# Performance work log

Measured on AMD Instinct MI355X. Metric: run time of the kernel, lower is better.

The kernel has to match this reference:

```python
import jax, jax.numpy as jnp
import numpy as np

BIG = 1e6  # diagonal mask value from the original module


def setup_inputs() -> dict:
    key = jax.random.key(0)
    k1, k2, k3 = jax.random.split(key, 3)
    B, D = 16384, 128
    return {
        "query_embeddings": jax.random.normal(k1, (B, D), dtype=jnp.float32),
        "doc_embeddings": jax.random.normal(k2, (B, D), dtype=jnp.float32),
        "neg_doc_embeddings": jax.random.normal(k3, (B, D), dtype=jnp.float32),
    }


def reference(query_embeddings, doc_embeddings, neg_doc_embeddings):
    # Pairwise term: diagonal of q @ d.T is just a row-wise dot product.
    pos_scores = jnp.einsum("bd,bd->b", query_embeddings, doc_embeddings)
    neg_scores = jnp.einsum("bd,bd->b", query_embeddings, neg_doc_embeddings)
    loss = jax.nn.softplus(neg_scores - pos_scores).mean()

    # In-batch hardest-negative term (in_batch_term=True): full [B, B] scores.
    scores = jnp.einsum("bd,cd->bc", query_embeddings, doc_embeddings)
    B = scores.shape[0]
    idx = jnp.arange(B)
    pos_ib = scores[idx, idx]
    # subtract 1e6 on the diagonal (same as original: scores - eye * 1e6)
    neg_ib = scores.at[idx, idx].add(-BIG).max(axis=1)
    loss = loss + jax.nn.softplus(neg_ib - pos_ib).mean()

    return loss / 2
```

## Files before the change

### kernel.cpp

```cpp
#include <hip/hip_runtime.h>
#include <hip/hip_bf16.h>


#define BATCH 16384
#define DDIM  128
#define NWAVES 8
#define ROWS_PER_BLOCK 512
#define COLS_PER_BLOCK 2048
#define CHUNK_COLS 128
#define NCHUNKS (COLS_PER_BLOCK / CHUNK_COLS)
#define CHUNK_USHORTS (CHUNK_COLS * DDIM)
#define NCG (BATCH / COLS_PER_BLOCK)

typedef __attribute__((ext_vector_type(8))) short bf16x8;
typedef __attribute__((ext_vector_type(4))) float f32x4;

__device__ __forceinline__ float softplus_f(float x) {
    return (x > 0.0f) ? x + log1pf(expf(-x)) : log1pf(expf(x));
}

__device__ __forceinline__ ushort f2bf_rne(float x) {
    unsigned u = __float_as_uint(x);
    unsigned r = (u + 0x7FFFu + ((u >> 16) & 1u)) >> 16;
    return (ushort)r;
}

#define WAITVM(n) do { \
        __builtin_amdgcn_s_waitcnt((n) | (7 << 4) | (15 << 8)); \
        asm volatile("" ::: "memory"); \
    } while (0)

__global__ __launch_bounds__(256) void prep_kernel(
    const float* __restrict__ q, const float* __restrict__ d,
    const float* __restrict__ nd,
    ushort* __restrict__ qb, ushort* __restrict__ db,
    float* __restrict__ pos, float* __restrict__ acc)
{
    const int t   = threadIdx.x;
    const int blk = blockIdx.x;
    const int sub = t >> 5;
    const int ln  = t & 31;
    const size_t base = (size_t)blk * (64 * DDIM);

    float loss1 = 0.0f;
#pragma unroll
    for (int i = 0; i < 8; ++i) {
        size_t idx = base + (size_t)i * 1024 + (size_t)t * 4;
        float4 a = *(const float4*)(q  + idx);
        float4 b = *(const float4*)(d  + idx);
        float4 c = *(const float4*)(nd + idx);

        ushort4 o;
        o.x = f2bf_rne(a.x); o.y = f2bf_rne(a.y);
        o.z = f2bf_rne(a.z); o.w = f2bf_rne(a.w);
        *(ushort4*)(qb + idx) = o;
        ushort4 p;
        p.x = f2bf_rne(b.x); p.y = f2bf_rne(b.y);
        p.z = f2bf_rne(b.z); p.w = f2bf_rne(b.w);
        *(ushort4*)(db + idx) = p;

        float ps = a.x * b.x + a.y * b.y + a.z * b.z + a.w * b.w;
        float ns = a.x * c.x + a.y * c.y + a.z * c.z + a.w * c.w;
        ps += __shfl_xor(ps, 1); ps += __shfl_xor(ps, 2);
        ps += __shfl_xor(ps, 4); ps += __shfl_xor(ps, 8);
        ps += __shfl_xor(ps, 16);
        ns += __shfl_xor(ns, 1); ns += __shfl_xor(ns, 2);
        ns += __shfl_xor(ns, 4); ns += __shfl_xor(ns, 8);
        ns += __shfl_xor(ns, 16);
        if (ln == 0) {
            int r = blk * 64 + i * 8 + sub;
            pos[r] = ps;
            loss1 += softplus_f(ns - ps);
        }
    }
    loss1 += __shfl_xor(loss1, 1);  loss1 += __shfl_xor(loss1, 2);
    loss1 += __shfl_xor(loss1, 4);  loss1 += __shfl_xor(loss1, 8);
    loss1 += __shfl_xor(loss1, 16); loss1 += __shfl_xor(loss1, 32);
    if ((t & 63) == 0) atomicAdd(acc, loss1);
}

__global__ __launch_bounds__(512, 2) void inbatch_kernel(
    const ushort* __restrict__ qb, const ushort* __restrict__ db,
    float* __restrict__ partials)
{
    __shared__ ushort stg[2][CHUNK_USHORTS];

    const int t      = threadIdx.x;
    const int w      = t >> 6;
    const int l      = t & 63;
    const int lane16 = l & 15;
    const int quad   = l >> 4;
    const int rg     = blockIdx.x & 31;
    const int cg     = blockIdx.x >> 5;
    const int rows0  = rg * ROWS_PER_BLOCK + w * 64;
    const int col0   = cg * COLS_PER_BLOCK;

    bf16x8 afrag[4][4];
#pragma unroll
    for (int rs = 0; rs < 4; ++rs)
#pragma unroll
        for (int ks = 0; ks < 4; ++ks)
            afrag[rs][ks] = *(const bf16x8*)(
                qb + (size_t)(rows0 + rs * 16 + lane16) * DDIM + ks * 32 + quad * 8);

    const ushort* gsrc[4];
#pragma unroll
    for (int i = 0; i < 4; ++i) {
        int seg = i * 512 + t;
        int c   = seg >> 4;
        int s   = seg & 15;
        gsrc[i] = db + (size_t)(col0 + c) * DDIM + ((s ^ (c & 15)) * 8);
    }

    int dsbase[4];
#pragma unroll
    for (int ks = 0; ks < 4; ++ks)
        dsbase[ks] = lane16 * DDIM + (((ks * 4 + quad) ^ lane16) * 8);

    float runmax[4][4];
#pragma unroll
    for (int rs = 0; rs < 4; ++rs)
#pragma unroll
        for (int r = 0; r < 4; ++r) runmax[rs][r] = -3.0e38f;

#pragma unroll
    for (int i = 0; i < 4; ++i)
        __builtin_amdgcn_global_load_lds(
            (const __attribute__((address_space(1))) void*)gsrc[i],
            (__attribute__((address_space(3))) void*)(&stg[0][0] + (i * 512 + w * 64) * 8),
            16, 0, 0);

    for (int ch = 0; ch < NCHUNKS; ++ch) {
        WAITVM(0);
        __syncthreads();
        if (ch + 1 < NCHUNKS) {
#pragma unroll
            for (int i = 0; i < 4; ++i)
                __builtin_amdgcn_global_load_lds(
                    (const __attribute__((address_space(1))) void*)(gsrc[i] + (size_t)(ch + 1) * CHUNK_USHORTS),
                    (__attribute__((address_space(3))) void*)(&stg[(ch + 1) & 1][0] + (i * 512 + w * 64) * 8),
                    16, 0, 0);
        }

        const ushort* buf = &stg[ch & 1][0];
#pragma unroll
        for (int ct = 0; ct < 8; ++ct) {
            bf16x8 bfrag[4];
#pragma unroll
            for (int ks = 0; ks < 4; ++ks)
                bfrag[ks] = *(const bf16x8*)(buf + dsbase[ks] + ct * 2048);

            const int ctile = col0 + ch * CHUNK_COLS + ct * 16;
#pragma unroll
            for (int rs = 0; rs < 4; ++rs) {
                f32x4 s = {0.0f, 0.0f, 0.0f, 0.0f};
#pragma unroll
                for (int ks = 0; ks < 4; ++ks)
                    s = __builtin_amdgcn_mfma_f32_16x16x32_bf16(
                        afrag[rs][ks], bfrag[ks], s, 0, 0, 0);
                if (ctile == rows0 + rs * 16) {
#pragma unroll
                    for (int r = 0; r < 4; ++r)
                        if (quad * 4 + r == lane16) s[r] -= 1.0e6f;
                }
#pragma unroll
                for (int r = 0; r < 4; ++r)
                    runmax[rs][r] = fmaxf(runmax[rs][r], s[r]);
            }
        }
    }

#pragma unroll
    for (int rs = 0; rs < 4; ++rs)
#pragma unroll
        for (int r = 0; r < 4; ++r) {
            float m = runmax[rs][r];
            m = fmaxf(m, __shfl_xor(m, 1));
            m = fmaxf(m, __shfl_xor(m, 2));
            m = fmaxf(m, __shfl_xor(m, 4));
            m = fmaxf(m, __shfl_xor(m, 8));
            runmax[rs][r] = m;
        }

    if (lane16 == 0) {
#pragma unroll
        for (int rs = 0; rs < 4; ++rs)
#pragma unroll
            for (int r = 0; r < 4; ++r)
                partials[(size_t)cg * BATCH + rows0 + rs * 16 + quad * 4 + r] =
                    runmax[rs][r];
    }
}

__global__ __launch_bounds__(256) void reduce_kernel(
    const float* __restrict__ partials, const float* __restrict__ pos,
    float* __restrict__ acc)
{
    const int r = blockIdx.x * 256 + threadIdx.x;
    float fm = partials[r];
#pragma unroll
    for (int cgi = 1; cgi < NCG; ++cgi)
        fm = fmaxf(fm, partials[(size_t)cgi * BATCH + r]);
    float c = softplus_f(fm - pos[r]);
    c += __shfl_xor(c, 1);  c += __shfl_xor(c, 2);
    c += __shfl_xor(c, 4);  c += __shfl_xor(c, 8);
    c += __shfl_xor(c, 16); c += __shfl_xor(c, 32);
    if ((threadIdx.x & 63) == 0) atomicAdd(acc + 1, c);
}

__global__ void finalize_kernel(const float* __restrict__ acc,
                                float* __restrict__ out)
{
    out[0] = (acc[0] + acc[1]) * (1.0f / (2.0f * BATCH));
}

extern "C" void kernel_launch(void* const* d_in, const int* in_sizes, int n_in,
                              void* d_out, int out_size, void* d_ws, size_t ws_size,
                              hipStream_t stream)
{
    const float* q  = (const float*)d_in[0];
    const float* d  = (const float*)d_in[1];
    const float* nd = (const float*)d_in[2];
    float* out = (float*)d_out;

    char* ws = (char*)d_ws;
    float*  acc      = (float*)ws;
    float*  pos      = (float*)(ws + 256);
    ushort* qb       = (ushort*)(ws + 256 + 65536);
    ushort* db       = (ushort*)(ws + 256 + 65536 + 4194304);
    float*  partials = (float*)(ws + 256 + 65536 + 2 * 4194304);

    hipMemsetAsync(acc, 0, 8, stream);
    prep_kernel<<<BATCH / 64, 256, 0, stream>>>(q, d, nd, qb, db, pos, acc);
    inbatch_kernel<<<(BATCH / ROWS_PER_BLOCK) * NCG, 512, 0, stream>>>(qb, db, partials);
    reduce_kernel<<<BATCH / 256, 256, 0, stream>>>(partials, pos, acc);
    finalize_kernel<<<1, 1, 0, stream>>>(acc, out);
}
```

Measured before the change: 141.6 us.

## Halve column tile, raise occupancy bound, replace atomics with partial-sum reductions

Halves the columns per in-batch block, doubling the block count, and raises launch bounds to four blocks per CU. The prep kernel now processes one row per 32-lane group across more blocks and writes per-block partial sums instead of atomics. The memset is removed, and finalize performs a parallel reduction of the prep and reduce partials. Capping occupancy higher may force register pressure or spills in the MFMA kernel, and LDS size may limit actual residency.

```diff
diff --git a/kernel.cpp b/kernel.cpp
--- a/kernel.cpp
+++ b/kernel.cpp
@@ -6,11 +6,13 @@
 #define DDIM  128
 #define NWAVES 8
 #define ROWS_PER_BLOCK 512
-#define COLS_PER_BLOCK 2048
+#define COLS_PER_BLOCK 1024
 #define CHUNK_COLS 128
 #define NCHUNKS (COLS_PER_BLOCK / CHUNK_COLS)
 #define CHUNK_USHORTS (CHUNK_COLS * DDIM)
 #define NCG (BATCH / COLS_PER_BLOCK)
+#define NPREP 2048
+#define NRED  64
 
 typedef __attribute__((ext_vector_type(8))) short bf16x8;
 typedef __attribute__((ext_vector_type(4))) float f32x4;
@@ -34,52 +36,51 @@
     const float* __restrict__ q, const float* __restrict__ d,
     const float* __restrict__ nd,
     ushort* __restrict__ qb, ushort* __restrict__ db,
-    float* __restrict__ pos, float* __restrict__ acc)
+    float* __restrict__ pos, float* __restrict__ loss1_part)
 {
     const int t   = threadIdx.x;
-    const int blk = blockIdx.x;
     const int sub = t >> 5;
     const int ln  = t & 31;
-    const size_t base = (size_t)blk * (64 * DDIM);
-
-    float loss1 = 0.0f;
-#pragma unroll
-    for (int i = 0; i < 8; ++i) {
-        size_t idx = base + (size_t)i * 1024 + (size_t)t * 4;
-        float4 a = *(const float4*)(q  + idx);
-        float4 b = *(const float4*)(d  + idx);
-        float4 c = *(const float4*)(nd + idx);
-
-        ushort4 o;
-        o.x = f2bf_rne(a.x); o.y = f2bf_rne(a.y);
-        o.z = f2bf_rne(a.z); o.w = f2bf_rne(a.w);
-        *(ushort4*)(qb + idx) = o;
-        ushort4 p;
-        p.x = f2bf_rne(b.x); p.y = f2bf_rne(b.y);
-        p.z = f2bf_rne(b.z); p.w = f2bf_rne(b.w);
-        *(ushort4*)(db + idx) = p;
-
-        float ps = a.x * b.x + a.y * b.y + a.z * b.z + a.w * b.w;
-        float ns = a.x * c.x + a.y * c.y + a.z * c.z + a.w * c.w;
-        ps += __shfl_xor(ps, 1); ps += __shfl_xor(ps, 2);
-        ps += __shfl_xor(ps, 4); ps += __shfl_xor(ps, 8);
-        ps += __shfl_xor(ps, 16);
-        ns += __shfl_xor(ns, 1); ns += __shfl_xor(ns, 2);
-        ns += __shfl_xor(ns, 4); ns += __shfl_xor(ns, 8);
-        ns += __shfl_xor(ns, 16);
-        if (ln == 0) {
-            int r = blk * 64 + i * 8 + sub;
-            pos[r] = ps;
-            loss1 += softplus_f(ns - ps);
-        }
-    }
-    loss1 += __shfl_xor(loss1, 1);  loss1 += __shfl_xor(loss1, 2);
-    loss1 += __shfl_xor(loss1, 4);  loss1 += __shfl_xor(loss1, 8);
-    loss1 += __shfl_xor(loss1, 16); loss1 += __shfl_xor(loss1, 32);
-    if ((t & 63) == 0) atomicAdd(acc, loss1);
-}
-
-__global__ __launch_bounds__(512, 2) void inbatch_kernel(
+    const int row = blockIdx.x * 8 + sub;
+    const size_t idx = (size_t)row * DDIM + ln * 4;
+
+    float4 a = *(const float4*)(q  + idx);
+    float4 b = *(const float4*)(d  + idx);
+    float4 c = *(const float4*)(nd + idx);
+
+    ushort4 o;
+    o.x = f2bf_rne(a.x); o.y = f2bf_rne(a.y);
+    o.z = f2bf_rne(a.z); o.w = f2bf_rne(a.w);
+    *(ushort4*)(qb + idx) = o;
+    ushort4 p;
+    p.x = f2bf_rne(b.x); p.y = f2bf_rne(b.y);
+    p.z = f2bf_rne(b.z); p.w = f2bf_rne(b.w);
+    *(ushort4*)(db + idx) = p;
+
+    float ps = a.x * b.x + a.y * b.y + a.z * b.z + a.w * b.w;
+    float ns = a.x * c.x + a.y * c.y + a.z * c.z + a.w * c.w;
+    ps += __shfl_xor(ps, 1); ps += __shfl_xor(ps, 2);
+    ps += __shfl_xor(ps, 4); ps += __shfl_xor(ps, 8);
+    ps += __shfl_xor(ps, 16);
+    ns += __shfl_xor(ns, 1); ns += __shfl_xor(ns, 2);
+    ns += __shfl_xor(ns, 4); ns += __shfl_xor(ns, 8);
+    ns += __shfl_xor(ns, 16);
+
+    float contrib = 0.0f;
+    if (ln == 0) {
+        pos[row] = ps;
+        contrib = softplus_f(ns - ps);
+    }
+    contrib += __shfl_xor(contrib, 32);
+
+    __shared__ float red[4];
+    if ((t & 63) == 0) red[t >> 6] = contrib;
+    __syncthreads();
+    if (t == 0)
+        loss1_part[blockIdx.x] = red[0] + red[1] + red[2] + red[3];
+}
+
+__global__ __launch_bounds__(512, 4) void inbatch_kernel(
     const ushort* __restrict__ qb, const ushort* __restrict__ db,
     float* __restrict__ partials)
 {
@@ -194,9 +195,10 @@
 
 __global__ __launch_bounds__(256) void reduce_kernel(
     const float* __restrict__ partials, const float* __restrict__ pos,
-    float* __restrict__ acc)
-{
-    const int r = blockIdx.x * 256 + threadIdx.x;
+    float* __restrict__ red_part)
+{
+    const int t = threadIdx.x;
+    const int r = blockIdx.x * 256 + t;
     float fm = partials[r];
 #pragma unroll
     for (int cgi = 1; cgi < NCG; ++cgi)
@@ -205,13 +207,33 @@
     c += __shfl_xor(c, 1);  c += __shfl_xor(c, 2);
     c += __shfl_xor(c, 4);  c += __shfl_xor(c, 8);
     c += __shfl_xor(c, 16); c += __shfl_xor(c, 32);
-    if ((threadIdx.x & 63) == 0) atomicAdd(acc + 1, c);
-}
-
-__global__ void finalize_kernel(const float* __restrict__ acc,
-                                float* __restrict__ out)
-{
-    out[0] = (acc[0] + acc[1]) * (1.0f / (2.0f * BATCH));
+
+    __shared__ float red[4];
+    if ((t & 63) == 0) red[t >> 6] = c;
+    __syncthreads();
+    if (t == 0)
+        red_part[blockIdx.x] = red[0] + red[1] + red[2] + red[3];
+}
+
+__global__ __launch_bounds__(256) void finalize_kernel(
+    const float* __restrict__ loss1_part, const float* __restrict__ red_part,
+    float* __restrict__ out)
+{
+    const int t = threadIdx.x;
+    float s = 0.0f;
+#pragma unroll
+    for (int i = 0; i < NPREP / 256; ++i)
+        s += loss1_part[i * 256 + t];
+    if (t < NRED) s += red_part[t];
+    s += __shfl_xor(s, 1);  s += __shfl_xor(s, 2);
+    s += __shfl_xor(s, 4);  s += __shfl_xor(s, 8);
+    s += __shfl_xor(s, 16); s += __shfl_xor(s, 32);
+
+    __shared__ float red[4];
+    if ((t & 63) == 0) red[t >> 6] = s;
+    __syncthreads();
+    if (t == 0)
+        out[0] = (red[0] + red[1] + red[2] + red[3]) * (1.0f / (2.0f * BATCH));
 }
 
 extern "C" void kernel_launch(void* const* d_in, const int* in_sizes, int n_in,
@@ -224,15 +246,15 @@
     float* out = (float*)d_out;
 
     char* ws = (char*)d_ws;
-    float*  acc      = (float*)ws;
-    float*  pos      = (float*)(ws + 256);
-    ushort* qb       = (ushort*)(ws + 256 + 65536);
-    ushort* db       = (ushort*)(ws + 256 + 65536 + 4194304);
-    float*  partials = (float*)(ws + 256 + 65536 + 2 * 4194304);
-
-    hipMemsetAsync(acc, 0, 8, stream);
-    prep_kernel<<<BATCH / 64, 256, 0, stream>>>(q, d, nd, qb, db, pos, acc);
+    float*  pos        = (float*)ws;
+    ushort* qb         = (ushort*)(ws + 65536);
+    ushort* db         = (ushort*)(ws + 65536 + 4194304);
+    float*  partials   = (float*)(ws + 65536 + 2 * 4194304);
+    float*  loss1_part = (float*)(ws + 65536 + 2 * 4194304 + 1048576);
+    float*  red_part   = (float*)(ws + 65536 + 2 * 4194304 + 1048576 + 8192);
+
+    prep_kernel<<<NPREP, 256, 0, stream>>>(q, d, nd, qb, db, pos, loss1_part);
     inbatch_kernel<<<(BATCH / ROWS_PER_BLOCK) * NCG, 512, 0, stream>>>(qb, db, partials);
-    reduce_kernel<<<BATCH / 256, 256, 0, stream>>>(partials, pos, acc);
-    finalize_kernel<<<1, 1, 0, stream>>>(acc, out);
-}
+    reduce_kernel<<<NRED, 256, 0, stream>>>(partials, pos, red_part);
+    finalize_kernel<<<1, 256, 0, stream>>>(loss1_part, red_part, out);
+}
```

Result: slower. 489.4 us (+245.6%).
